# Kernel tuning notes

Measured on AMD Instinct MI355X. Metric: run time of the kernel, lower is better.

Reference implementation:

```python
import jax, jax.numpy as jnp
import numpy as np
from jax import lax

SAMPLES = 1024  # matches init kwarg samples=1024


def setup_inputs() -> dict:
    key = jax.random.key(0)
    inputs = jax.random.normal(key, (4, 8192, 3), dtype=jnp.float32)  # B,N,3 point cloud
    return {"inputs": inputs}


def _dist_to(points, sel):
    # points: (B,N,3), sel: (B,3) -> (B,N) euclidean distance (same math as tf.norm on t1-t2)
    return jnp.linalg.norm(points - sel[:, None, :], axis=-1)


def reference(inputs):
    # Faithful FPS: original forms full BxNxN dist matrix; the math only ever
    # uses one row per iteration, so we compute rows on the fly (identical values).
    points = inputs  # (B,N,3)

    # ds initialized to distances from point 0 (row 0 of the dist matrix)
    ds = _dist_to(points, points[:, 0, :])  # (B,N)

    # first sample: argmax of ds, then min-update
    idx0 = jnp.argmax(ds, axis=-1)  # (B,)
    sel0 = jnp.take_along_axis(points, idx0[:, None, None], axis=1)[:, 0, :]  # (B,3)
    ds = jnp.minimum(ds, _dist_to(points, sel0))

    def step(ds, _):
        idx = jnp.argmax(ds, axis=-1)  # (B,)
        sel = jnp.take_along_axis(points, idx[:, None, None], axis=1)[:, 0, :]  # (B,3)
        ds = jnp.minimum(ds, _dist_to(points, sel))
        return ds, sel

    _, sels = lax.scan(step, ds, None, length=SAMPLES - 1)  # sels: (S-1,B,3)
    sampled = jnp.concatenate([sel0[:, None, :], jnp.transpose(sels, (1, 0, 2))], axis=1)
    return sampled  # (B,SAMPLES,3)
```

## Files before the change

kernel.cpp:

```cpp
#include <hip/hip_runtime.h>
#include <cfloat>
#include <cmath>


#define NPTS 8192
#define NSAMP 1024
#define TPB 256
#define PPT (NPTS / TPB)
#define NW (TPB / 64)

#define KEY_MERGE(CTRL)                                                               \
    do {                                                                              \
        const unsigned th = (unsigned)__builtin_amdgcn_update_dpp(0, (int)kh, (CTRL), 0xF, 0xF, true); \
        const unsigned tl = (unsigned)__builtin_amdgcn_update_dpp(0, (int)kl, (CTRL), 0xF, 0xF, true); \
        const unsigned long long tk = ((unsigned long long)th << 32) | tl;            \
        const unsigned long long pk = ((unsigned long long)kh << 32) | kl;            \
        const bool take = tk > pk;                                                    \
        kh = take ? th : kh;                                                          \
        kl = take ? tl : kl;                                                          \
    } while (0)

__global__ __launch_bounds__(TPB, 1) void fps_kernel(const float* __restrict__ pts,
                                                     float* __restrict__ out) {
#pragma clang fp contract(off)
    const int b = blockIdx.x;
    const int tid = threadIdx.x;
    const float* __restrict__ P = pts + (size_t)b * NPTS * 3;
    float* __restrict__ O = out + (size_t)b * NSAMP * 3;

    __shared__ float4 sp4[NPTS];
    __shared__ float  sOut[NSAMP * 3];
    __shared__ __align__(16) uint2 sSlot[2][NW];

    float px[PPT], py[PPT], pz[PPT], dsq[PPT];

    const float p0x = P[0], p0y = P[1], p0z = P[2];

    float mval = -FLT_MAX, m2 = -FLT_MAX;
    int mj = 0;
#pragma unroll
    for (int j = 0; j < PPT; ++j) {
        const int i = j * TPB + tid;
        const float x = P[i * 3 + 0];
        const float y = P[i * 3 + 1];
        const float z = P[i * 3 + 2];
        px[j] = x; py[j] = y; pz[j] = z;
        sp4[i] = make_float4(x, y, z, 0.0f);
        const float dx = x - p0x, dy = y - p0y, dz = z - p0z;
        const float d = (dx * dx + dy * dy) + dz * dz;
        dsq[j] = d;
        const float t = fminf(d, mval);
        m2 = fmaxf(m2, t);
        if (d > mval) { mval = d; mj = j; }
    }
    __syncthreads();

    const int lane = tid & 63;
    const int wid  = tid >> 6;

    for (int s = 0; s < NSAMP; ++s) {
        const int buf = s & 1;

        const float sU = sqrtf(mval);
        if (m2 >= mval * 0.999999f) {
#pragma unroll
            for (int j = PPT - 1; j >= 0; --j)
                if (sqrtf(dsq[j]) == sU) mj = j;
        }
        unsigned kh = __float_as_uint(sU);
        unsigned kl = ~(unsigned)(mj * TPB + tid);

        KEY_MERGE(0x111);
        KEY_MERGE(0x112);
        KEY_MERGE(0x114);
        KEY_MERGE(0x118);
        KEY_MERGE(0x142);
        KEY_MERGE(0x143);
        if (lane == 63) sSlot[buf][wid] = make_uint2(kl, kh);
        __syncthreads();

        const uint4* sl = reinterpret_cast<const uint4*>(&sSlot[buf][0]);
        const uint4 a = sl[0];
        const uint4 c4 = sl[1];
        const unsigned long long K0 = ((unsigned long long)a.y  << 32) | a.x;
        const unsigned long long K1 = ((unsigned long long)a.w  << 32) | a.z;
        const unsigned long long K2 = ((unsigned long long)c4.y << 32) | c4.x;
        const unsigned long long K3 = ((unsigned long long)c4.w << 32) | c4.z;
        const unsigned long long m01 = K0 > K1 ? K0 : K1;
        const unsigned long long m23 = K2 > K3 ? K2 : K3;
        const unsigned long long K   = m01 > m23 ? m01 : m23;

        const int gidx = (int)(~(unsigned)K);
        const float4 c = sp4[gidx];
        const float sx = c.x, sy = c.y, sz = c.z;

        if (tid == 0) {
            sOut[s * 3 + 0] = sx;
            sOut[s * 3 + 1] = sy;
            sOut[s * 3 + 2] = sz;
        }

        mval = -FLT_MAX; m2 = -FLT_MAX; mj = 0;
#pragma unroll
        for (int j = 0; j < PPT; ++j) {
            const float dx = px[j] - sx;
            const float dy = py[j] - sy;
            const float dz = pz[j] - sz;
            const float nd = (dx * dx + dy * dy) + dz * dz;
            const float d  = fminf(dsq[j], nd);
            dsq[j] = d;
            const float t = fminf(d, mval);
            m2 = fmaxf(m2, t);
            if (d > mval) { mval = d; mj = j; }
        }
    }

    __syncthreads();
#pragma unroll
    for (int k = tid; k < NSAMP * 3; k += TPB)
        O[k] = sOut[k];
}

extern "C" void kernel_launch(void* const* d_in, const int* in_sizes, int n_in,
                              void* d_out, int out_size, void* d_ws, size_t ws_size,
                              hipStream_t stream) {
    const float* pts = (const float*)d_in[0];
    float* out = (float*)d_out;
    const int B = in_sizes[0] / (NPTS * 3);
    fps_kernel<<<B, TPB, 0, stream>>>(pts, out);
}
```

Before: 1.152 ms.

## Reduce max value only, then resolve argmax index via shared atomicMin

The per-point inner loop now tracks only a running max of squared distances instead of max, second max and the argmax index, which leaves fewer per-point instructions. The cross-lane reduction works on a single 32-bit value rather than a 64-bit key, halving the DPP work. Only the threads whose local max matches the block max then search their registers for the index and publish it with a shared atomicMin. This costs an extra __syncthreads per sample and a divergent search in the winning threads.

```diff
diff --git a/kernel.cpp b/kernel.cpp
--- a/kernel.cpp
+++ b/kernel.cpp
@@ -9,16 +9,7 @@
 #define PPT (NPTS / TPB)
 #define NW (TPB / 64)
 
-#define KEY_MERGE(CTRL)                                                               \
-    do {                                                                              \
-        const unsigned th = (unsigned)__builtin_amdgcn_update_dpp(0, (int)kh, (CTRL), 0xF, 0xF, true); \
-        const unsigned tl = (unsigned)__builtin_amdgcn_update_dpp(0, (int)kl, (CTRL), 0xF, 0xF, true); \
-        const unsigned long long tk = ((unsigned long long)th << 32) | tl;            \
-        const unsigned long long pk = ((unsigned long long)kh << 32) | kl;            \
-        const bool take = tk > pk;                                                    \
-        kh = take ? th : kh;                                                          \
-        kl = take ? tl : kl;                                                          \
-    } while (0)
+__device__ __forceinline__ unsigned umax2(unsigned a, unsigned b) { return a > b ? a : b; }
 
 __global__ __launch_bounds__(TPB, 1) void fps_kernel(const float* __restrict__ pts,
                                                      float* __restrict__ out) {
@@ -30,28 +21,33 @@
 
     __shared__ float4 sp4[NPTS];
     __shared__ float  sOut[NSAMP * 3];
-    __shared__ __align__(16) uint2 sSlot[2][NW];
+    __shared__ __align__(16) unsigned sMax[NW];
+    __shared__ unsigned sIdx[2];
 
     float px[PPT], py[PPT], pz[PPT], dsq[PPT];
 
     const float p0x = P[0], p0y = P[1], p0z = P[2];
+    if (tid == 0) { sIdx[0] = 0xFFFFFFFFu; sIdx[1] = 0xFFFFFFFFu; }
 
-    float mval = -FLT_MAX, m2 = -FLT_MAX;
-    int mj = 0;
+    float tmax = 0.0f;
 #pragma unroll
-    for (int j = 0; j < PPT; ++j) {
-        const int i = j * TPB + tid;
-        const float x = P[i * 3 + 0];
-        const float y = P[i * 3 + 1];
-        const float z = P[i * 3 + 2];
-        px[j] = x; py[j] = y; pz[j] = z;
-        sp4[i] = make_float4(x, y, z, 0.0f);
-        const float dx = x - p0x, dy = y - p0y, dz = z - p0z;
-        const float d = (dx * dx + dy * dy) + dz * dz;
-        dsq[j] = d;
-        const float t = fminf(d, mval);
-        m2 = fmaxf(m2, t);
-        if (d > mval) { mval = d; mj = j; }
+    for (int jj = 0; jj < PPT; jj += 2) {
+        float d01[2];
+#pragma unroll
+        for (int k = 0; k < 2; ++k) {
+            const int j = jj + k;
+            const int i = j * TPB + tid;
+            const float x = P[i * 3 + 0];
+            const float y = P[i * 3 + 1];
+            const float z = P[i * 3 + 2];
+            px[j] = x; py[j] = y; pz[j] = z;
+            sp4[i] = make_float4(x, y, z, 0.0f);
+            const float dx = x - p0x, dy = y - p0y, dz = z - p0z;
+            const float d = (dx * dx + dy * dy) + dz * dz;
+            dsq[j] = d;
+            d01[k] = d;
+        }
+        tmax = fmaxf(tmax, fmaxf(d01[0], d01[1]));
     }
     __syncthreads();
 
@@ -61,36 +57,42 @@
     for (int s = 0; s < NSAMP; ++s) {
         const int buf = s & 1;
 
-        const float sU = sqrtf(mval);
-        if (m2 >= mval * 0.999999f) {
-#pragma unroll
-            for (int j = PPT - 1; j >= 0; --j)
-                if (sqrtf(dsq[j]) == sU) mj = j;
-        }
-        unsigned kh = __float_as_uint(sU);
-        unsigned kl = ~(unsigned)(mj * TPB + tid);
-
-        KEY_MERGE(0x111);
-        KEY_MERGE(0x112);
-        KEY_MERGE(0x114);
-        KEY_MERGE(0x118);
-        KEY_MERGE(0x142);
-        KEY_MERGE(0x143);
-        if (lane == 63) sSlot[buf][wid] = make_uint2(kl, kh);
+        unsigned v = __float_as_uint(tmax), t;
+        t = (unsigned)__builtin_amdgcn_update_dpp(0, (int)v, 0x111, 0xF, 0xF, true); v = umax2(v, t);
+        t = (unsigned)__builtin_amdgcn_update_dpp(0, (int)v, 0x112, 0xF, 0xF, true); v = umax2(v, t);
+        t = (unsigned)__builtin_amdgcn_update_dpp(0, (int)v, 0x114, 0xF, 0xF, true); v = umax2(v, t);
+        t = (unsigned)__builtin_amdgcn_update_dpp(0, (int)v, 0x118, 0xF, 0xF, true); v = umax2(v, t);
+        t = (unsigned)__builtin_amdgcn_update_dpp(0, (int)v, 0x142, 0xF, 0xF, true); v = umax2(v, t);
+        t = (unsigned)__builtin_amdgcn_update_dpp(0, (int)v, 0x143, 0xF, 0xF, true); v = umax2(v, t);
+        if (lane == 63) sMax[wid] = v;
         __syncthreads();
 
-        const uint4* sl = reinterpret_cast<const uint4*>(&sSlot[buf][0]);
-        const uint4 a = sl[0];
-        const uint4 c4 = sl[1];
-        const unsigned long long K0 = ((unsigned long long)a.y  << 32) | a.x;
-        const unsigned long long K1 = ((unsigned long long)a.w  << 32) | a.z;
-        const unsigned long long K2 = ((unsigned long long)c4.y << 32) | c4.x;
-        const unsigned long long K3 = ((unsigned long long)c4.w << 32) | c4.z;
-        const unsigned long long m01 = K0 > K1 ? K0 : K1;
-        const unsigned long long m23 = K2 > K3 ? K2 : K3;
-        const unsigned long long K   = m01 > m23 ? m01 : m23;
+        const uint4 sv = *reinterpret_cast<const uint4*>(sMax);
+        const unsigned M = umax2(umax2(sv.x, sv.y), umax2(sv.z, sv.w));
+        const float U   = sqrtf(__uint_as_float(M));
+        const float myU = sqrtf(tmax);
 
-        const int gidx = (int)(~(unsigned)K);
+        if (tid == 0) sIdx[buf ^ 1] = 0xFFFFFFFFu;
+
+        if (myU == U) {
+            unsigned cj = 0u;
+            bool nt = false;
+            const float thr = tmax * 0.999999f;
+#pragma unroll
+            for (int j = PPT - 1; j >= 0; --j) {
+                nt |= (dsq[j] >= thr) & (__float_as_uint(dsq[j]) != __float_as_uint(tmax));
+                if (__float_as_uint(dsq[j]) == __float_as_uint(tmax)) cj = (unsigned)j;
+            }
+            if (nt) {
+#pragma unroll
+                for (int j = PPT - 1; j >= 0; --j)
+                    if (sqrtf(dsq[j]) == U) cj = (unsigned)j;
+            }
+            atomicMin(&sIdx[buf], cj * TPB + (unsigned)tid);
+        }
+        __syncthreads();
+
+        const int gidx = (int)sIdx[buf];
         const float4 c = sp4[gidx];
         const float sx = c.x, sy = c.y, sz = c.z;
 
@@ -100,18 +102,22 @@
             sOut[s * 3 + 2] = sz;
         }
 
-        mval = -FLT_MAX; m2 = -FLT_MAX; mj = 0;
+        tmax = 0.0f;
 #pragma unroll
-        for (int j = 0; j < PPT; ++j) {
-            const float dx = px[j] - sx;
-            const float dy = py[j] - sy;
-            const float dz = pz[j] - sz;
-            const float nd = (dx * dx + dy * dy) + dz * dz;
-            const float d  = fminf(dsq[j], nd);
-            dsq[j] = d;
-            const float t = fminf(d, mval);
-            m2 = fmaxf(m2, t);
-            if (d > mval) { mval = d; mj = j; }
+        for (int jj = 0; jj < PPT; jj += 2) {
+            float d01[2];
+#pragma unroll
+            for (int k = 0; k < 2; ++k) {
+                const int j = jj + k;
+                const float dx = px[j] - sx;
+                const float dy = py[j] - sy;
+                const float dz = pz[j] - sz;
+                const float nd = (dx * dx + dy * dy) + dz * dz;
+                const float d  = fminf(dsq[j], nd);
+                dsq[j] = d;
+                d01[k] = d;
+            }
+            tmax = fmaxf(tmax, fmaxf(d01[0], d01[1]));
         }
     }
 
```

New measurement: 1.582 ms. 1.37x slower.
